# Optimization experiments

Measured on AMD Instinct MI355X. Metric: run time of the kernel, lower is better.

Reference implementation:

```python
import jax, jax.numpy as jnp
import numpy as np

# Module hyperparameters (init_kwargs)
N_CODES = 1024    # context_size
Q_LEN = 8         # query_len
D_MODEL = 256     # d_model
BATCH = 16384
DECAY = 0.99
EPSILON = 1e-05


def setup_inputs() -> dict:
    key = jax.random.key(0)
    k1, k2, k3 = jax.random.split(key, 3)
    q = jax.random.normal(k1, (BATCH, Q_LEN, D_MODEL), jnp.float32)
    context = jax.random.normal(k2, (N_CODES, Q_LEN, D_MODEL), jnp.float32)
    ema_count = jnp.ones((N_CODES,), jnp.float32)
    ema_dw = jax.random.normal(k3, (N_CODES, Q_LEN, D_MODEL), jnp.float32) * 0.1
    return {"q": q, "context": context, "ema_count": ema_count, "ema_dw": ema_dw}


def _forward(q, context, ema_count, ema_dw):
    B, Q, D = q.shape
    N = context.shape[0]
    q_flat = q.reshape(B, Q * D)              # [B, QD]
    g_flat = context.reshape(N, Q * D)        # [N, QD]
    Dflat = Q * D

    # squared-euclidean cdist via the matmul expansion, then nearest code
    distances = (jnp.sum(q_flat * q_flat, axis=1, keepdims=True)
                 + jnp.sum(g_flat * g_flat, axis=1)
                 - 2.0 * (q_flat @ g_flat.T))                      # [B, N]
    indices = jnp.argmin(distances, axis=-1)                       # [B]

    # einsum('bn,nqd->bqd', one_hot, context) == gather
    q_context = context[indices]                                   # [B, Q, D]
    # einsum('bn,bqd->nqd', one_hot, q) == scatter-add by code id
    q_hat = jax.ops.segment_sum(q, indices, num_segments=N)        # [N, Q, D]

    # per-sample mean MSE (q_context detached in original)
    qld = jnp.mean((jax.lax.stop_gradient(q_context) - q) ** 2, axis=(1, 2))  # [B]

    # EMA codebook update (training mode, no-grad in original)
    counts = jax.ops.segment_sum(jnp.ones((B,), q.dtype), indices, num_segments=N)  # [N]
    ec = DECAY * ema_count + (1.0 - DECAY) * counts
    n = jnp.sum(ec)
    ec = (ec + EPSILON) / (n + Dflat * EPSILON) * n                # Laplace smoothing
    edw = DECAY * ema_dw + (1.0 - DECAY) * jax.lax.stop_gradient(q_hat)
    context_new = edw / ec[:, None, None]                          # [N, Q, D]

    # straight-through output uses the UPDATED (detached) context
    out_context = (q_hat + jax.lax.stop_gradient(context_new - q_hat)).reshape(-1, D)  # [N*Q, D]
    return qld, out_context, ec, edw, context_new


def reference(q, context, ema_count, ema_dw):
    return _forward(q, context, ema_count, ema_dw)
```

## Files before the change

kernel.cpp:

```cpp
#include <hip/hip_runtime.h>
#include <hip/hip_bf16.h>
#include <float.h>

#define BSZ 16384
#define NCODES 1024
#define QD 2048
#define NCHUNK 64
#define NCOLG 16

typedef _Float16 f16x8 __attribute__((ext_vector_type(8)));
typedef _Float16 f16x4 __attribute__((ext_vector_type(4)));
typedef float f32x4 __attribute__((ext_vector_type(4)));

static __device__ __forceinline__ float one_minus_decay() { return (float)(1.0 - 0.99); }

static __device__ __forceinline__ void async_copy16(const void* src, void* lds) {
    __builtin_amdgcn_global_load_lds((const __attribute__((address_space(1))) void*)src,
                                     (__attribute__((address_space(3))) void*)lds, 16, 0, 0);
}

__global__ void k_prep_all(const float* __restrict__ ctx, const float* __restrict__ q,
                           _Float16* __restrict__ gh, float* __restrict__ gsq,
                           _Float16* __restrict__ qh, float* __restrict__ qsq) {
    __shared__ float red[4];
    int tid = threadIdx.x;
    const float* src; _Float16* dh; float* nrm;
    if (blockIdx.x < NCODES) {
        size_t n = blockIdx.x;
        src = ctx + n * QD; dh = gh + n * QD; nrm = gsq + n;
    } else {
        size_t b = blockIdx.x - NCODES;
        src = q + b * QD; dh = qh + b * QD; nrm = qsq + b;
    }
    int c = tid * 8;
    float4 t0 = *(const float4*)(src + c);
    float4 t1 = *(const float4*)(src + c + 4);
    float s = t0.x * t0.x + t0.y * t0.y + t0.z * t0.z + t0.w * t0.w
            + t1.x * t1.x + t1.y * t1.y + t1.z * t1.z + t1.w * t1.w;
    f16x8 h;
    h[0] = (_Float16)t0.x; h[1] = (_Float16)t0.y;
    h[2] = (_Float16)t0.z; h[3] = (_Float16)t0.w;
    h[4] = (_Float16)t1.x; h[5] = (_Float16)t1.y;
    h[6] = (_Float16)t1.z; h[7] = (_Float16)t1.w;
    *(f16x8*)(dh + c) = h;
    for (int off = 32; off > 0; off >>= 1) s += __shfl_down(s, off);
    if ((tid & 63) == 0) red[tid >> 6] = s;
    __syncthreads();
    if (tid == 0) *nrm = red[0] + red[1] + red[2] + red[3];
}

__global__ void k_prep_r17(const float* __restrict__ ctx, const float* __restrict__ q,
                           _Float16* __restrict__ gh, float* __restrict__ gsq,
                           float* __restrict__ qsq) {
    int tid = threadIdx.x;
    if (blockIdx.x < NCODES) {
        __shared__ float red[4];
        int n = blockIdx.x;
        float s = 0.f;
#pragma unroll
        for (int i = 0; i < 2; ++i) {
            int c = (tid + i * 256) * 4;
            float4 t = *(const float4*)(ctx + (size_t)n * QD + c);
            f16x4 h;
            h[0] = (_Float16)t.x; h[1] = (_Float16)t.y;
            h[2] = (_Float16)t.z; h[3] = (_Float16)t.w;
            *(f16x4*)(gh + (size_t)n * QD + c) = h;
            s += t.x * t.x + t.y * t.y + t.z * t.z + t.w * t.w;
        }
        for (int off = 32; off > 0; off >>= 1) s += __shfl_down(s, off);
        if ((tid & 63) == 0) red[tid >> 6] = s;
        __syncthreads();
        if (tid == 0) gsq[n] = red[0] + red[1] + red[2] + red[3];
    } else {
        int w = tid >> 6, lane = tid & 63;
        int b = (blockIdx.x - NCODES) * 4 + w;
        const float4* row = (const float4*)(q + (size_t)b * QD);
        float s = 0.f;
#pragma unroll
        for (int i = 0; i < 8; ++i) {
            float4 v = row[lane + i * 64];
            s += v.x * v.x + v.y * v.y + v.z * v.z + v.w * v.w;
        }
        for (int off = 32; off > 0; off >>= 1) s += __shfl_down(s, off);
        if (lane == 0) qsq[b] = s;
    }
}

__launch_bounds__(256)
__global__ void k_dist_pre(const _Float16* __restrict__ qh, const _Float16* __restrict__ gh,
                           const float* __restrict__ gsq,
                           float* __restrict__ pval, int* __restrict__ pidx) {
    __shared__ _Float16 ah[2][128][64];
    __shared__ _Float16 bh[2][128][64];

    const int tid = threadIdx.x;
    const int lane = tid & 63, wid = tid >> 6;
    const int wr = wid >> 1, wc = wid & 1;
    const int n0 = blockIdx.x;
    const int xcd = n0 & 7, j = n0 >> 3;
    const int col = j & 7, rowt = xcd * 16 + (j >> 3);
    const int colBase = col * 128, rowBase = rowt * 128;
    const int fr = lane & 15, kg = lane >> 4;

    const int srow = lane >> 3;
    const int gran = (lane & 7) ^ (lane >> 3);

    f32x4 acc[4][4];
#pragma unroll
    for (int m = 0; m < 4; ++m)
#pragma unroll
        for (int n = 0; n < 4; ++n) acc[m][n] = (f32x4)0.f;

    for (int kb = 0; kb < QD; kb += 128) {
        __syncthreads();
#pragma unroll
        for (int d = 0; d < 2; ++d) {
#pragma unroll
            for (int i = 0; i < 4; ++i) {
                int g = wid * 4 + i;
                size_t roff = (size_t)(rowBase + g * 8 + srow) * QD + kb + d * 64 + gran * 8;
                size_t coff = (size_t)(colBase + g * 8 + srow) * QD + kb + d * 64 + gran * 8;
                async_copy16(qh + roff, &ah[d][g * 8][0]);
                async_copy16(gh + coff, &bh[d][g * 8][0]);
            }
        }
        __syncthreads();

#pragma unroll
        for (int d = 0; d < 2; ++d) {
            const char* ahB = (const char*)&ah[d][0][0];
            const char* bhB = (const char*)&bh[d][0][0];
#pragma unroll
            for (int h = 0; h < 2; ++h) {
                f16x8 a_h[4], b_h[4];
#pragma unroll
                for (int m = 0; m < 4; ++m) {
                    int ar = wr * 64 + m * 16 + fr;
                    int off = ar * 128 + ((h * 64 + kg * 16) ^ ((ar & 7) << 4));
                    a_h[m] = *(const f16x8*)(ahB + off);
                }
#pragma unroll
                for (int n = 0; n < 4; ++n) {
                    int br = wc * 64 + n * 16 + fr;
                    int off = br * 128 + ((h * 64 + kg * 16) ^ ((br & 7) << 4));
                    b_h[n] = *(const f16x8*)(bhB + off);
                }
#pragma unroll
                for (int m = 0; m < 4; ++m)
#pragma unroll
                    for (int n = 0; n < 4; ++n)
                        acc[m][n] = __builtin_amdgcn_mfma_f32_16x16x32_f16(a_h[m], b_h[n], acc[m][n], 0, 0, 0);
            }
        }
    }

    float mv[4][4]; int mi[4][4];
#pragma unroll
    for (int m = 0; m < 4; ++m)
#pragma unroll
        for (int r = 0; r < 4; ++r) { mv[m][r] = FLT_MAX; mi[m][r] = 0x7fffffff; }
#pragma unroll
    for (int n = 0; n < 4; ++n) {
        int c = colBase + wc * 64 + n * 16 + fr;
        float gq = gsq[c];
#pragma unroll
        for (int m = 0; m < 4; ++m)
#pragma unroll
            for (int r = 0; r < 4; ++r) {
                float d = gq - 2.0f * acc[m][n][r];
                if (d < mv[m][r]) { mv[m][r] = d; mi[m][r] = c; }
            }
    }
#pragma unroll
    for (int off = 1; off < 16; off <<= 1) {
#pragma unroll
        for (int m = 0; m < 4; ++m)
#pragma unroll
            for (int r = 0; r < 4; ++r) {
                float ov = __shfl_xor(mv[m][r], off);
                int   oi = __shfl_xor(mi[m][r], off);
                if (ov < mv[m][r] || (ov == mv[m][r] && oi < mi[m][r])) { mv[m][r] = ov; mi[m][r] = oi; }
            }
    }
    if (fr == 0) {
        const size_t slot = (size_t)(col * 2 + wc) * BSZ;
#pragma unroll
        for (int m = 0; m < 4; ++m)
#pragma unroll
            for (int r = 0; r < 4; ++r) {
                int grow = rowBase + wr * 64 + m * 16 + kg * 4 + r;
                pval[slot + grow] = mv[m][r];
                pidx[slot + grow] = mi[m][r];
            }
    }
}

__launch_bounds__(256)
__global__ void k_dist_r17(const float* __restrict__ q, const _Float16* __restrict__ gh,
                           const float* __restrict__ gsq,
                           float* __restrict__ pval, int* __restrict__ pidx) {
    __shared__ _Float16 ah[128][64];
    __shared__ _Float16 bh[128][64];

    const int tid = threadIdx.x;
    const int lane = tid & 63, wid = tid >> 6;
    const int wr = wid >> 1, wc = wid & 1;
    const int n0 = blockIdx.x;
    const int xcd = n0 & 7, j = n0 >> 3;
    const int col = j & 7, rowt = xcd * 16 + (j >> 3);
    const int colBase = col * 128, rowBase = rowt * 128;
    const int fr = lane & 15, kg = lane >> 4;

    char* ahB = (char*)&ah[0][0];
    const char* bhB = (const char*)&bh[0][0];

    f32x4 acc[4][4];
#pragma unroll
    for (int m = 0; m < 4; ++m)
#pragma unroll
        for (int n = 0; n < 4; ++n) acc[m][n] = (f32x4)0.f;

    for (int kb = 0; kb < QD; kb += 64) {
        __syncthreads();
#pragma unroll
        for (int s = 0; s < 8; ++s) {
            int f = s * 256 + tid;
            int row = f >> 4, k4 = (f & 15) * 4;
            float4 t = *(const float4*)(q + (size_t)(rowBase + row) * QD + kb + k4);
            f16x4 h;
            h[0] = (_Float16)t.x; h[1] = (_Float16)t.y;
            h[2] = (_Float16)t.z; h[3] = (_Float16)t.w;
            int byt = (row * 128 + k4 * 2) ^ ((row & 7) << 4);
            *(f16x4*)(ahB + byt) = h;
        }
#pragma unroll
        for (int i = 0; i < 4; ++i) {
            int g = wid * 4 + i;
            int row = g * 8 + (lane >> 3);
            int gran = (lane & 7) ^ (lane >> 3);
            size_t goff = (size_t)(colBase + row) * QD + kb + gran * 8;
            async_copy16(gh + goff, &bh[g * 8][0]);
        }
        __syncthreads();

#pragma unroll
        for (int h = 0; h < 2; ++h) {
            f16x8 a_h[4], b_h[4];
#pragma unroll
            for (int m = 0; m < 4; ++m) {
                int ar = wr * 64 + m * 16 + fr;
                int off = ar * 128 + ((h * 64 + kg * 16) ^ ((ar & 7) << 4));
                a_h[m] = *(const f16x8*)(ahB + off);
            }
#pragma unroll
            for (int n = 0; n < 4; ++n) {
                int br = wc * 64 + n * 16 + fr;
                int off = br * 128 + ((h * 64 + kg * 16) ^ ((br & 7) << 4));
                b_h[n] = *(const f16x8*)(bhB + off);
            }
#pragma unroll
            for (int m = 0; m < 4; ++m)
#pragma unroll
                for (int n = 0; n < 4; ++n)
                    acc[m][n] = __builtin_amdgcn_mfma_f32_16x16x32_f16(a_h[m], b_h[n], acc[m][n], 0, 0, 0);
        }
    }

    float mv[4][4]; int mi[4][4];
#pragma unroll
    for (int m = 0; m < 4; ++m)
#pragma unroll
        for (int r = 0; r < 4; ++r) { mv[m][r] = FLT_MAX; mi[m][r] = 0x7fffffff; }
#pragma unroll
    for (int n = 0; n < 4; ++n) {
        int c = colBase + wc * 64 + n * 16 + fr;
        float gq = gsq[c];
#pragma unroll
        for (int m = 0; m < 4; ++m)
#pragma unroll
            for (int r = 0; r < 4; ++r) {
                float d = gq - 2.0f * acc[m][n][r];
                if (d < mv[m][r]) { mv[m][r] = d; mi[m][r] = c; }
            }
    }
#pragma unroll
    for (int off = 1; off < 16; off <<= 1) {
#pragma unroll
        for (int m = 0; m < 4; ++m)
#pragma unroll
            for (int r = 0; r < 4; ++r) {
                float ov = __shfl_xor(mv[m][r], off);
                int   oi = __shfl_xor(mi[m][r], off);
                if (ov < mv[m][r] || (ov == mv[m][r] && oi < mi[m][r])) { mv[m][r] = ov; mi[m][r] = oi; }
            }
    }
    if (fr == 0) {
        const size_t slot = (size_t)(col * 2 + wc) * BSZ;
#pragma unroll
        for (int m = 0; m < 4; ++m)
#pragma unroll
            for (int r = 0; r < 4; ++r) {
                int grow = rowBase + wr * 64 + m * 16 + kg * 4 + r;
                pval[slot + grow] = mv[m][r];
                pidx[slot + grow] = mi[m][r];
            }
    }
}

__global__ void k_merge(const float* __restrict__ pval, const int* __restrict__ pidx,
                        const float* __restrict__ qsq,
                        int* __restrict__ idx_out, float* __restrict__ qld,
                        int* __restrict__ chunkhist) {
    __shared__ int h[NCODES];
    int c = blockIdx.x, tid = threadIdx.x;
    int b = c * 256 + tid;
#pragma unroll
    for (int s = 0; s < 4; ++s) h[tid + s * 256] = 0;
    float bv = pval[b]; int bi = pidx[b];
    for (int y = 1; y < NCOLG; ++y) {
        float v = pval[(size_t)y * BSZ + b]; int ii = pidx[(size_t)y * BSZ + b];
        if (v < bv || (v == bv && ii < bi)) { bv = v; bi = ii; }
    }
    idx_out[b] = bi;
    qld[b] = (qsq[b] + bv) * (1.0f / (float)QD);
    __syncthreads();
    atomicAdd(&h[bi], 1);
    __syncthreads();
#pragma unroll
    for (int s = 0; s < 4; ++s) chunkhist[c * NCODES + tid + s * 256] = h[tid + s * 256];
}

__global__ void k_scan(const int* __restrict__ chunkhist, int* __restrict__ base,
                       int* __restrict__ counts, int* __restrict__ offsets,
                       const float* __restrict__ ema_count, float* __restrict__ ec_out) {
    __shared__ int s[NCODES];
    __shared__ float e2[NCODES];
    int code = threadIdx.x;
    int run = 0;
    for (int c = 0; c < NCHUNK; ++c) {
        base[c * NCODES + code] = run;
        run += chunkhist[c * NCODES + code];
    }
    counts[code] = run;
    s[code] = run; __syncthreads();
    for (int off = 1; off < NCODES; off <<= 1) {
        int v = (code >= off) ? s[code - off] : 0;
        __syncthreads();
        s[code] += v; __syncthreads();
    }
    offsets[code] = s[code] - run;
    float er = 0.99f * ema_count[code] + one_minus_decay() * (float)run;
    e2[code] = er; __syncthreads();
    for (int off = 512; off > 0; off >>= 1) {
        if (code < off) e2[code] += e2[code + off];
        __syncthreads();
    }
    float n = e2[0];
    ec_out[code] = (er + 1e-5f) / (n + (float)(2048.0 * 1e-5)) * n;
}

__global__ void k_fill(const int* __restrict__ idx, const int* __restrict__ base,
                       const int* __restrict__ offsets, int* __restrict__ list) {
    __shared__ int sidx[256];
    int c = blockIdx.x, tid = threadIdx.x;
    int b = c * 256 + tid;
    int n = idx[b];
    sidx[tid] = n; __syncthreads();
    int rank = 0;
    for (int j = 0; j < tid; ++j) rank += (sidx[j] == n);
    list[offsets[n] + base[c * NCODES + n] + rank] = b;
}

__global__ void k_qhat_h(const _Float16* __restrict__ qh, const int* __restrict__ counts,
                         const int* __restrict__ offsets, const int* __restrict__ list,
                         float* __restrict__ qhat) {
    int n = blockIdx.x;
    int col = blockIdx.y * 256 + threadIdx.x;
    int cnt = counts[n];
    const int* lp = list + offsets[n];
    float a0 = 0.f, a1 = 0.f, a2 = 0.f, a3 = 0.f, a4 = 0.f, a5 = 0.f, a6 = 0.f, a7 = 0.f;
    int i = 0;
    for (; i + 8 <= cnt; i += 8) {
        int b0 = lp[i], b1 = lp[i + 1], b2 = lp[i + 2], b3 = lp[i + 3];
        int b4 = lp[i + 4], b5 = lp[i + 5], b6 = lp[i + 6], b7 = lp[i + 7];
        a0 += (float)qh[(size_t)b0 * QD + col]; a1 += (float)qh[(size_t)b1 * QD + col];
        a2 += (float)qh[(size_t)b2 * QD + col]; a3 += (float)qh[(size_t)b3 * QD + col];
        a4 += (float)qh[(size_t)b4 * QD + col]; a5 += (float)qh[(size_t)b5 * QD + col];
        a6 += (float)qh[(size_t)b6 * QD + col]; a7 += (float)qh[(size_t)b7 * QD + col];
    }
    for (; i < cnt; ++i) a0 += (float)qh[(size_t)lp[i] * QD + col];
    float r = ((a0 + a1) + (a2 + a3)) + ((a4 + a5) + (a6 + a7));
    qhat[(size_t)n * QD + col] = r;
}

__global__ void k_qhat_f(const float* __restrict__ q, const int* __restrict__ counts,
                         const int* __restrict__ offsets, const int* __restrict__ list,
                         float* __restrict__ qhat) {
    int n = blockIdx.x;
    int col = blockIdx.y * 256 + threadIdx.x;
    int cnt = counts[n];
    const int* lp = list + offsets[n];
    float a0 = 0.f, a1 = 0.f, a2 = 0.f, a3 = 0.f, a4 = 0.f, a5 = 0.f, a6 = 0.f, a7 = 0.f;
    int i = 0;
    for (; i + 8 <= cnt; i += 8) {
        int b0 = lp[i], b1 = lp[i + 1], b2 = lp[i + 2], b3 = lp[i + 3];
        int b4 = lp[i + 4], b5 = lp[i + 5], b6 = lp[i + 6], b7 = lp[i + 7];
        a0 += q[(size_t)b0 * QD + col]; a1 += q[(size_t)b1 * QD + col];
        a2 += q[(size_t)b2 * QD + col]; a3 += q[(size_t)b3 * QD + col];
        a4 += q[(size_t)b4 * QD + col]; a5 += q[(size_t)b5 * QD + col];
        a6 += q[(size_t)b6 * QD + col]; a7 += q[(size_t)b7 * QD + col];
    }
    for (; i < cnt; ++i) a0 += q[(size_t)lp[i] * QD + col];
    float r = ((a0 + a1) + (a2 + a3)) + ((a4 + a5) + (a6 + a7));
    qhat[(size_t)n * QD + col] = r;
}

__global__ void k_fin(const float* __restrict__ ema_dw, const float* __restrict__ ec,
                      const float* qhat, float* edw_out, float* ctxnew_out,
                      float* outctx_out) {
    size_t i = ((size_t)blockIdx.x * 256 + threadIdx.x) * 8;
    int n = (int)(i >> 11);
    float e = ec[n];
    float om = one_minus_decay();
#pragma unroll
    for (int h = 0; h < 2; ++h) {
        float4 dw = *(const float4*)(ema_dw + i + h * 4);
        float4 qh = *(const float4*)(qhat + i + h * 4);
        float4 ed, cn;
        ed.x = 0.99f * dw.x + om * qh.x; ed.y = 0.99f * dw.y + om * qh.y;
        ed.z = 0.99f * dw.z + om * qh.z; ed.w = 0.99f * dw.w + om * qh.w;
        cn.x = ed.x / e; cn.y = ed.y / e; cn.z = ed.z / e; cn.w = ed.w / e;
        *(float4*)(edw_out + i + h * 4) = ed;
        *(float4*)(ctxnew_out + i + h * 4) = cn;
        *(float4*)(outctx_out + i + h * 4) = cn;
    }
}

extern "C" void kernel_launch(void* const* d_in, const int* in_sizes, int n_in,
                              void* d_out, int out_size, void* d_ws, size_t ws_size,
                              hipStream_t stream) {
    const float* q         = (const float*)d_in[0];
    const float* ctx       = (const float*)d_in[1];
    const float* ema_count = (const float*)d_in[2];
    const float* ema_dw    = (const float*)d_in[3];

    float* out = (float*)d_out;
    float* o_qld    = out;
    float* o_outctx = out + BSZ;
    float* o_ec     = o_outctx + (size_t)NCODES * QD;
    float* o_edw    = o_ec + NCODES;
    float* o_ctxnew = o_edw + (size_t)NCODES * QD;

    char* w = (char*)d_ws;
    float* ws_gsq   = (float*)w;
    int* ws_idx     = (int*)(w + 4096);
    int* ws_counts  = (int*)(w + 4096 + 65536);
    int* ws_offsets = ws_counts + NCODES;
    int* ws_list    = ws_offsets + NCODES;

    const size_t presplit_need = (size_t)1048576 + (size_t)BSZ * QD * sizeof(_Float16);
    const bool use_pre = (ws_size >= presplit_need);
    _Float16* qh = (_Float16*)(w + 1048576);

    _Float16* gh = (_Float16*)o_ctxnew;
    float* pval  = o_edw;
    int*   pidx  = (int*)(o_edw + (size_t)NCOLG * BSZ);
    float* qsq   = o_edw + (size_t)2 * NCOLG * BSZ;
    int* chunkhist = (int*)o_outctx;
    int* basep     = chunkhist + NCHUNK * NCODES;
    float* qhat    = o_outctx;

    if (use_pre) {
        k_prep_all<<<NCODES + BSZ, 256, 0, stream>>>(ctx, q, gh, ws_gsq, qh, qsq);
        k_dist_pre<<<1024, 256, 0, stream>>>(qh, gh, ws_gsq, pval, pidx);
    } else {
        k_prep_r17<<<NCODES + BSZ / 4, 256, 0, stream>>>(ctx, q, gh, ws_gsq, qsq);
        k_dist_r17<<<1024, 256, 0, stream>>>(q, gh, ws_gsq, pval, pidx);
    }
    k_merge <<<NCHUNK, 256, 0, stream>>>(pval, pidx, qsq, ws_idx, o_qld, chunkhist);
    k_scan  <<<1, 1024, 0, stream>>>(chunkhist, basep, ws_counts, ws_offsets, ema_count, o_ec);
    k_fill  <<<NCHUNK, 256, 0, stream>>>(ws_idx, basep, ws_offsets, ws_list);
    if (use_pre) {
        k_qhat_h<<<dim3(NCODES, 8), 256, 0, stream>>>(qh, ws_counts, ws_offsets, ws_list, qhat);
    } else {
        k_qhat_f<<<dim3(NCODES, 8), 256, 0, stream>>>(q, ws_counts, ws_offsets, ws_list, qhat);
    }
    k_fin   <<<NCODES * QD / 2048, 256, 0, stream>>>(ema_dw, o_ec, qhat,
                                                     o_edw, o_ctxnew, o_outctx);
}
```

Measured before the change: 200.9 us.

## Double-buffer the distance GEMM K-loop with async LDS prefetch

Replaces the load-all-then-compute K loop, which did two 64-wide sub-tiles per 128 step behind full barriers, with a two-stage ring of 64-wide K tiles. The next tile is staged while the current one is computed, and `s_waitcnt vmcnt(8)` waits only for the older stage. This is meant to hide global-to-LDS latency behind MFMA work in the main distance matmul. It relies on the vmcnt accounting matching the eight async loads issued per stage, and it adds an explicit barrier before buffer reuse.

After: 199.7 us. About the same (-0.6%).

```diff
diff --git a/kernel.cpp b/kernel.cpp
--- a/kernel.cpp
+++ b/kernel.cpp
@@ -111,48 +111,62 @@
 #pragma unroll
         for (int n = 0; n < 4; ++n) acc[m][n] = (f32x4)0.f;
 
-    for (int kb = 0; kb < QD; kb += 128) {
-        __syncthreads();
-#pragma unroll
-        for (int d = 0; d < 2; ++d) {
-#pragma unroll
-            for (int i = 0; i < 4; ++i) {
-                int g = wid * 4 + i;
-                size_t roff = (size_t)(rowBase + g * 8 + srow) * QD + kb + d * 64 + gran * 8;
-                size_t coff = (size_t)(colBase + g * 8 + srow) * QD + kb + d * 64 + gran * 8;
-                async_copy16(qh + roff, &ah[d][g * 8][0]);
-                async_copy16(gh + coff, &bh[d][g * 8][0]);
-            }
-        }
-        __syncthreads();
-
-#pragma unroll
-        for (int d = 0; d < 2; ++d) {
-            const char* ahB = (const char*)&ah[d][0][0];
-            const char* bhB = (const char*)&bh[d][0][0];
-#pragma unroll
-            for (int h = 0; h < 2; ++h) {
-                f16x8 a_h[4], b_h[4];
-#pragma unroll
-                for (int m = 0; m < 4; ++m) {
-                    int ar = wr * 64 + m * 16 + fr;
-                    int off = ar * 128 + ((h * 64 + kg * 16) ^ ((ar & 7) << 4));
-                    a_h[m] = *(const f16x8*)(ahB + off);
-                }
-#pragma unroll
-                for (int n = 0; n < 4; ++n) {
-                    int br = wc * 64 + n * 16 + fr;
-                    int off = br * 128 + ((h * 64 + kg * 16) ^ ((br & 7) << 4));
-                    b_h[n] = *(const f16x8*)(bhB + off);
-                }
-#pragma unroll
-                for (int m = 0; m < 4; ++m)
-#pragma unroll
-                    for (int n = 0; n < 4; ++n)
-                        acc[m][n] = __builtin_amdgcn_mfma_f32_16x16x32_f16(a_h[m], b_h[n], acc[m][n], 0, 0, 0);
-            }
-        }
-    }
+#define STAGE_TILE(KB, BUF)                                                           \
+    {                                                                                 \
+        _Pragma("unroll")                                                             \
+        for (int i_ = 0; i_ < 4; ++i_) {                                              \
+            int g_ = wid * 4 + i_;                                                    \
+            size_t ro_ = (size_t)(rowBase + g_ * 8 + srow) * QD + (KB) + gran * 8;    \
+            size_t co_ = (size_t)(colBase + g_ * 8 + srow) * QD + (KB) + gran * 8;    \
+            async_copy16(qh + ro_, &ah[BUF][g_ * 8][0]);                              \
+            async_copy16(gh + co_, &bh[BUF][g_ * 8][0]);                              \
+        }                                                                             \
+    }
+
+#define COMPUTE_TILE(BUF)                                                             \
+    {                                                                                 \
+        const char* ahB_ = (const char*)&ah[BUF][0][0];                               \
+        const char* bhB_ = (const char*)&bh[BUF][0][0];                               \
+        _Pragma("unroll")                                                             \
+        for (int h_ = 0; h_ < 2; ++h_) {                                              \
+            f16x8 a_h[4], b_h[4];                                                     \
+            _Pragma("unroll")                                                         \
+            for (int m_ = 0; m_ < 4; ++m_) {                                          \
+                int ar_ = wr * 64 + m_ * 16 + fr;                                     \
+                int off_ = ar_ * 128 + ((h_ * 64 + kg * 16) ^ ((ar_ & 7) << 4));      \
+                a_h[m_] = *(const f16x8*)(ahB_ + off_);                               \
+            }                                                                         \
+            _Pragma("unroll")                                                         \
+            for (int n_ = 0; n_ < 4; ++n_) {                                          \
+                int br_ = wc * 64 + n_ * 16 + fr;                                     \
+                int off_ = br_ * 128 + ((h_ * 64 + kg * 16) ^ ((br_ & 7) << 4));      \
+                b_h[n_] = *(const f16x8*)(bhB_ + off_);                               \
+            }                                                                         \
+            _Pragma("unroll")                                                         \
+            for (int m_ = 0; m_ < 4; ++m_)                                            \
+                _Pragma("unroll")                                                     \
+                for (int n_ = 0; n_ < 4; ++n_)                                        \
+                    acc[m_][n_] = __builtin_amdgcn_mfma_f32_16x16x32_f16(             \
+                        a_h[m_], b_h[n_], acc[m_][n_], 0, 0, 0);                      \
+        }                                                                             \
+    }
+
+    STAGE_TILE(0, 0);
+    STAGE_TILE(64, 1);
+
+    for (int t = 0; t < 31; ++t) {
+        asm volatile("s_waitcnt vmcnt(8)" ::: "memory");
+        __builtin_amdgcn_s_barrier();
+        COMPUTE_TILE(t & 1);
+        __builtin_amdgcn_s_barrier();
+        if (t < 30) STAGE_TILE((t + 2) * 64, t & 1);
+    }
+    asm volatile("s_waitcnt vmcnt(0)" ::: "memory");
+    __builtin_amdgcn_s_barrier();
+    COMPUTE_TILE(1);
+
+#undef STAGE_TILE
+#undef COMPUTE_TILE
 
     float mv[4][4]; int mi[4][4];
 #pragma unroll
```
